# Performance work log

Hardware: AMD Instinct MI355X
Metric: run time of the kernel (lower is better)

## Reference

```python
import jax, jax.numpy as jnp
import numpy as np

B, H_HIST, S_DIM, HID, G, K, A = 1024, 16384, 32, 64, 10, 4, 8


def setup_inputs() -> dict:
    key = jax.random.key(0)
    ks = jax.random.split(key, 12)
    inp = {
        'state_batch': jax.random.normal(ks[0], (B, S_DIM), jnp.float32),
        'state_history_batch': jax.random.normal(ks[1], (H_HIST, S_DIM), jnp.float32),
        'joint_action_history_batch': jax.random.normal(ks[2], (H_HIST, G, A), jnp.float32),
        # per-abstract-agent encoder MLP: Linear(S->H) + ReLU, Linear(H->H) + ReLU, Linear(H->H) + ReLU
        'W0': jax.random.normal(ks[3], (K, S_DIM, HID), jnp.float32) / np.sqrt(S_DIM),
        'b0': jax.random.normal(ks[4], (K, HID), jnp.float32) * 0.01,
        'W1': jax.random.normal(ks[5], (K, HID, HID), jnp.float32) / np.sqrt(HID),
        'b1': jax.random.normal(ks[6], (K, HID), jnp.float32) * 0.01,
        'W2': jax.random.normal(ks[7], (K, HID, HID), jnp.float32) / np.sqrt(HID),
        'b2': jax.random.normal(ks[8], (K, HID), jnp.float32) * 0.01,
        'assignment_matrix': jnp.ones((G, K), jnp.float32),
    }
    return inp


def _encode(x, W0, b0, W1, b1, W2, b2):
    # x: [N, S_DIM] shared across K encoders -> [K, N, HID]
    h = jax.nn.relu(jnp.einsum('ni,kio->kno', x, W0) + b0[:, None, :])
    h = jax.nn.relu(jnp.einsum('kni,kio->kno', h, W1) + b1[:, None, :])
    h = jax.nn.relu(jnp.einsum('kni,kio->kno', h, W2) + b2[:, None, :])
    return h


def reference(state_batch, state_history_batch, joint_action_history_batch,
              W0, b0, W1, b1, W2, b2, assignment_matrix):
    enc_s = _encode(state_batch, W0, b0, W1, b1, W2, b2)            # [K, B, HID]
    enc_h = _encode(state_history_batch, W0, b0, W1, b1, W2, b2)    # [K, H, HID]
    # per (abstract agent k, batch item b): softmax over history of <enc_h, enc_s>
    attn = jax.nn.softmax(jnp.einsum('khd,kbd->kbh', enc_h, enc_s), axis=-1)  # [K, B, H]
    # weighted action aggregation: [H,G,A] contracted over H
    abs_pred = jnp.einsum('kbh,hga->kbga', attn, joint_action_history_batch)  # [K, B, G, A]
    soft_assign = jax.nn.softmax(assignment_matrix, axis=-1)                  # [G, K]
    out = jnp.einsum('gk,kbga->bga', soft_assign, abs_pred)                   # [B, G, A]
    return out
```

## Files before the change

### kernel.cpp

```cpp
#include <hip/hip_runtime.h>
#include <stdint.h>

#define B_SZ 1024
#define H_SZ 16384
#define SD   32
#define HID  64
#define G_SZ 10
#define K_SZ 4
#define A_SZ 8
#define VA   80
#define NC   16
#define CH   (H_SZ/NC)

typedef float f32x4  __attribute__((ext_vector_type(4)));
typedef short bf16x8 __attribute__((ext_vector_type(8)));

__device__ inline short f2bf(float a) {
    unsigned u = __float_as_uint(a);
    return (short)((u + 0x7FFFu + ((u >> 16) & 1u)) >> 16);
}
__device__ inline float bf2f(short s) {
    return __uint_as_float(((unsigned)(unsigned short)s) << 16);
}
__device__ inline void split_bf(float v, short& hi, short& lo) {
    hi = f2bf(v);
    lo = f2bf(v - bf2f(hi));
}
__device__ inline int pk_bf16(float a, float b) {
    unsigned ua = __float_as_uint(a), ub = __float_as_uint(b);
    ua = (ua + 0x7FFFu + ((ua >> 16) & 1u)) >> 16;
    ub = (ub + 0x7FFFu + ((ub >> 16) & 1u)) >> 16;
    return (int)(ua | (ub << 16));
}

__global__ __launch_bounds__(256, 2) void k_encode(
    const float* __restrict__ state, const float* __restrict__ hist,
    const float* __restrict__ act,
    const float* __restrict__ W0, const float* __restrict__ b0,
    const float* __restrict__ W1, const float* __restrict__ b1,
    const float* __restrict__ W2, const float* __restrict__ b2,
    short* __restrict__ enc_s_h, short* __restrict__ enc_s_l,
    short* __restrict__ enc_h_h, short* __restrict__ enc_h_l,
    short* __restrict__ vt_h, short* __restrict__ vt_l)
{
    __shared__ __align__(16) short smem[28672];
    const int bid = blockIdx.x;
    const int t = threadIdx.x;

    if (bid >= 1088) {
        short* tile_h = smem;
        short* tile_l = smem + 10752;
        const int h0 = (bid - 1088) * 128;
        for (int i = 0; i < 40; ++i) {
            int idx = t + i * 256;
            float v = act[(size_t)h0 * VA + idx];
            int h = idx / VA, c = idx - h * VA;
            short hh, ll; split_bf(v, hh, ll);
            tile_h[h * 84 + c] = hh;
            tile_l[h * 84 + c] = ll;
        }
        __syncthreads();
        for (int i = 0; i < 5; ++i) {
            int j = t + i * 256;
            int va = j >> 4, hc = j & 15;
            union { short s[8]; uint4 v; } uh, ul;
            #pragma unroll
            for (int uu = 0; uu < 8; ++uu) {
                uh.s[uu] = tile_h[(hc * 8 + uu) * 84 + va];
                ul.s[uu] = tile_l[(hc * 8 + uu) * 84 + va];
            }
            *(uint4*)(vt_h + (size_t)va * H_SZ + h0 + hc * 8) = uh.v;
            *(uint4*)(vt_l + (size_t)va * H_SZ + h0 + hc * 8) = ul.v;
        }
        return;
    }

    const int k = bid / 272;
    const int tl = bid % 272;
    const float* X;
    short *dst_h, *dst_l;
    if (tl < 16) {
        X = state + (size_t)tl * 64 * SD;
        dst_h = enc_s_h + ((size_t)k * B_SZ + tl * 64) * HID;
        dst_l = enc_s_l + ((size_t)k * B_SZ + tl * 64) * HID;
    } else {
        X = hist + (size_t)(tl - 16) * 64 * SD;
        dst_h = enc_h_h + ((size_t)k * H_SZ + (tl - 16) * 64) * HID;
        dst_l = enc_h_l + ((size_t)k * H_SZ + (tl - 16) * 64) * HID;
    }

    short* xt_h  = smem;
    short* xt_l  = smem + 2560;
    short* wt0_h = smem + 5120;
    short* wt0_l = smem + 7680;
    short* hb2_h = smem;
    short* hb2_l = smem + 4608;
    short* wt1_h = smem + 10240;
    short* wt1_l = smem + 14848;
    short* hb1_h = smem + 19456;
    short* hb1_l = smem + 24064;
    short* wt2_h = smem + 19456;
    short* wt2_l = smem + 24064;

    const float* W0k = W0 + k * (SD * HID);
    const float* W1k = W1 + k * (HID * HID);
    const float* W2k = W2 + k * (HID * HID);

    {
        int r = t >> 2, c0 = (t & 3) * 8;
        const float* src = X + r * SD + c0;
        #pragma unroll
        for (int u = 0; u < 8; ++u) {
            short hh, ll; split_bf(src[u], hh, ll);
            xt_h[r * 40 + c0 + u] = hh;
            xt_l[r * 40 + c0 + u] = ll;
        }
    }
    {
        int i = t >> 3, j0 = (t & 7) * 8;
        #pragma unroll
        for (int u = 0; u < 8; ++u) {
            short hh, ll; split_bf(W0k[i * HID + j0 + u], hh, ll);
            wt0_h[(j0 + u) * 40 + i] = hh;
            wt0_l[(j0 + u) * 40 + i] = ll;
        }
    }
    {
        int i = t >> 2, j0 = (t & 3) * 16;
        #pragma unroll
        for (int u = 0; u < 16; ++u) {
            short hh, ll; split_bf(W1k[i * HID + j0 + u], hh, ll);
            wt1_h[(j0 + u) * 72 + i] = hh;
            wt1_l[(j0 + u) * 72 + i] = ll;
        }
    }
    __syncthreads();

    const int w = t >> 6, l15 = t & 15, quad = (t >> 4) & 3;
    const f32x4 fz = {0.f, 0.f, 0.f, 0.f};

    {
        bf16x8 xa_h = *(const bf16x8*)(xt_h + (w * 16 + l15) * 40 + quad * 8);
        bf16x8 xa_l = *(const bf16x8*)(xt_l + (w * 16 + l15) * 40 + quad * 8);
        const float* b0k = b0 + k * HID;
        #pragma unroll
        for (int tt = 0; tt < 4; ++tt) {
            bf16x8 wf_h = *(const bf16x8*)(wt0_h + (l15 + 16 * tt) * 40 + quad * 8);
            bf16x8 wf_l = *(const bf16x8*)(wt0_l + (l15 + 16 * tt) * 40 + quad * 8);
            f32x4 c = __builtin_amdgcn_mfma_f32_16x16x32_bf16(xa_h, wf_h, fz, 0, 0, 0);
            c = __builtin_amdgcn_mfma_f32_16x16x32_bf16(xa_l, wf_h, c, 0, 0, 0);
            c = __builtin_amdgcn_mfma_f32_16x16x32_bf16(xa_h, wf_l, c, 0, 0, 0);
            float bias = b0k[l15 + 16 * tt];
            #pragma unroll
            for (int r = 0; r < 4; ++r) {
                float f = fmaxf(c[r] + bias, 0.f);
                short hh, ll; split_bf(f, hh, ll);
                hb1_h[(w * 16 + quad * 4 + r) * 72 + l15 + 16 * tt] = hh;
                hb1_l[(w * 16 + quad * 4 + r) * 72 + l15 + 16 * tt] = ll;
            }
        }
    }
    __syncthreads();
    {
        bf16x8 ha0_h = *(const bf16x8*)(hb1_h + (w * 16 + l15) * 72 + quad * 8);
        bf16x8 ha0_l = *(const bf16x8*)(hb1_l + (w * 16 + l15) * 72 + quad * 8);
        bf16x8 ha1_h = *(const bf16x8*)(hb1_h + (w * 16 + l15) * 72 + 32 + quad * 8);
        bf16x8 ha1_l = *(const bf16x8*)(hb1_l + (w * 16 + l15) * 72 + 32 + quad * 8);
        const float* b1k = b1 + k * HID;
        #pragma unroll
        for (int tt = 0; tt < 4; ++tt) {
            bf16x8 wfa_h = *(const bf16x8*)(wt1_h + (l15 + 16 * tt) * 72 + quad * 8);
            bf16x8 wfa_l = *(const bf16x8*)(wt1_l + (l15 + 16 * tt) * 72 + quad * 8);
            bf16x8 wfb_h = *(const bf16x8*)(wt1_h + (l15 + 16 * tt) * 72 + 32 + quad * 8);
            bf16x8 wfb_l = *(const bf16x8*)(wt1_l + (l15 + 16 * tt) * 72 + 32 + quad * 8);
            f32x4 c = __builtin_amdgcn_mfma_f32_16x16x32_bf16(ha0_h, wfa_h, fz, 0, 0, 0);
            c = __builtin_amdgcn_mfma_f32_16x16x32_bf16(ha1_h, wfb_h, c, 0, 0, 0);
            c = __builtin_amdgcn_mfma_f32_16x16x32_bf16(ha0_l, wfa_h, c, 0, 0, 0);
            c = __builtin_amdgcn_mfma_f32_16x16x32_bf16(ha1_l, wfb_h, c, 0, 0, 0);
            c = __builtin_amdgcn_mfma_f32_16x16x32_bf16(ha0_h, wfa_l, c, 0, 0, 0);
            c = __builtin_amdgcn_mfma_f32_16x16x32_bf16(ha1_h, wfb_l, c, 0, 0, 0);
            float bias = b1k[l15 + 16 * tt];
            #pragma unroll
            for (int r = 0; r < 4; ++r) {
                float f = fmaxf(c[r] + bias, 0.f);
                short hh, ll; split_bf(f, hh, ll);
                hb2_h[(w * 16 + quad * 4 + r) * 72 + l15 + 16 * tt] = hh;
                hb2_l[(w * 16 + quad * 4 + r) * 72 + l15 + 16 * tt] = ll;
            }
        }
    }
    __syncthreads();
    {
        int i = t >> 2, j0 = (t & 3) * 16;
        #pragma unroll
        for (int u = 0; u < 16; ++u) {
            short hh, ll; split_bf(W2k[i * HID + j0 + u], hh, ll);
            wt2_h[(j0 + u) * 72 + i] = hh;
            wt2_l[(j0 + u) * 72 + i] = ll;
        }
    }
    __syncthreads();
    {
        bf16x8 ha0_h = *(const bf16x8*)(hb2_h + (w * 16 + l15) * 72 + quad * 8);
        bf16x8 ha0_l = *(const bf16x8*)(hb2_l + (w * 16 + l15) * 72 + quad * 8);
        bf16x8 ha1_h = *(const bf16x8*)(hb2_h + (w * 16 + l15) * 72 + 32 + quad * 8);
        bf16x8 ha1_l = *(const bf16x8*)(hb2_l + (w * 16 + l15) * 72 + 32 + quad * 8);
        const float* b2k = b2 + k * HID;
        #pragma unroll
        for (int tt = 0; tt < 4; ++tt) {
            bf16x8 wfa_h = *(const bf16x8*)(wt2_h + (l15 + 16 * tt) * 72 + quad * 8);
            bf16x8 wfa_l = *(const bf16x8*)(wt2_l + (l15 + 16 * tt) * 72 + quad * 8);
            bf16x8 wfb_h = *(const bf16x8*)(wt2_h + (l15 + 16 * tt) * 72 + 32 + quad * 8);
            bf16x8 wfb_l = *(const bf16x8*)(wt2_l + (l15 + 16 * tt) * 72 + 32 + quad * 8);
            f32x4 c = __builtin_amdgcn_mfma_f32_16x16x32_bf16(ha0_h, wfa_h, fz, 0, 0, 0);
            c = __builtin_amdgcn_mfma_f32_16x16x32_bf16(ha1_h, wfb_h, c, 0, 0, 0);
            c = __builtin_amdgcn_mfma_f32_16x16x32_bf16(ha0_l, wfa_h, c, 0, 0, 0);
            c = __builtin_amdgcn_mfma_f32_16x16x32_bf16(ha1_l, wfb_h, c, 0, 0, 0);
            c = __builtin_amdgcn_mfma_f32_16x16x32_bf16(ha0_h, wfa_l, c, 0, 0, 0);
            c = __builtin_amdgcn_mfma_f32_16x16x32_bf16(ha1_h, wfb_l, c, 0, 0, 0);
            float bias = b2k[l15 + 16 * tt];
            #pragma unroll
            for (int r = 0; r < 4; ++r) {
                float f = fmaxf(c[r] + bias, 0.f);
                short hh, ll; split_bf(f, hh, ll);
                dst_h[(w * 16 + quad * 4 + r) * HID + l15 + 16 * tt] = hh;
                dst_l[(w * 16 + quad * 4 + r) * HID + l15 + 16 * tt] = ll;
            }
        }
    }
}

__global__ __launch_bounds__(256, 2) void k_flash(
    const short* __restrict__ enc_s_h, const short* __restrict__ enc_s_l,
    const short* __restrict__ enc_h_h, const short* __restrict__ enc_h_l,
    const short* __restrict__ vth, const short* __restrict__ vtl,
    float* __restrict__ Pm, float* __restrict__ Pl, float* __restrict__ Pacc)
{
    __shared__ __align__(16) short kh_h[32 * 72];
    __shared__ __align__(16) short kh_l[32 * 72];
    __shared__ __align__(16) short vts_h[80 * 40];
    __shared__ __align__(16) short vts_l[80 * 40];

    const int bid = blockIdx.x;
    const int mtile = bid & 7, chunk = (bid >> 3) & 15, k = bid >> 7;
    const int t = threadIdx.x, w = t >> 6, l15 = t & 15, quad = (t >> 4) & 3;
    const short* ehk_h = enc_h_h + (size_t)k * H_SZ * HID;
    const short* ehk_l = enc_h_l + (size_t)k * H_SZ * HID;
    const int h_base = chunk * CH;
    const int q0 = mtile * 128 + w * 32;
    const float L2E = 1.44269504f;
    const f32x4 fz = {0.f, 0.f, 0.f, 0.f};

    bf16x8 qh[2][2], ql[2][2];
    #pragma unroll
    for (int sub = 0; sub < 2; ++sub)
        #pragma unroll
        for (int kb = 0; kb < 2; ++kb) {
            size_t off = ((size_t)k * B_SZ + q0 + sub * 16 + l15) * HID + kb * 32 + quad * 8;
            qh[sub][kb] = *(const bf16x8*)(enc_s_h + off);
            ql[sub][kb] = *(const bf16x8*)(enc_s_l + off);
        }

    f32x4 acc[2][5];
    #pragma unroll
    for (int s = 0; s < 2; ++s)
        #pragma unroll
        for (int tt = 0; tt < 5; ++tt) acc[s][tt] = fz;
    float mrun[2] = {-__builtin_inff(), -__builtin_inff()};
    float lrun[2] = {0.f, 0.f};

    const int krr = t >> 3, kcc = (t & 7) * 8;
    const int vrw = t >> 2, vcl = (t & 3) * 8;
    const int vrw2 = 64 + (t >> 2);

    uint4 pkh, pkl, pvh, pvl, pv2h, pv2l;
    auto load_tile = [&](int h0) {
        pkh = *(const uint4*)(ehk_h + (size_t)(h0 + krr) * HID + kcc);
        pkl = *(const uint4*)(ehk_l + (size_t)(h0 + krr) * HID + kcc);
        pvh = *(const uint4*)(vth + (size_t)vrw * H_SZ + h0 + vcl);
        pvl = *(const uint4*)(vtl + (size_t)vrw * H_SZ + h0 + vcl);
        if (t < 64) {
            pv2h = *(const uint4*)(vth + (size_t)vrw2 * H_SZ + h0 + vcl);
            pv2l = *(const uint4*)(vtl + (size_t)vrw2 * H_SZ + h0 + vcl);
        }
    };
    auto store_tile = [&]() {
        *(uint4*)(kh_h + krr * 72 + kcc) = pkh;
        *(uint4*)(kh_l + krr * 72 + kcc) = pkl;
        *(uint4*)(vts_h + vrw * 40 + vcl) = pvh;
        *(uint4*)(vts_l + vrw * 40 + vcl) = pvl;
        if (t < 64) {
            *(uint4*)(vts_h + vrw2 * 40 + vcl) = pv2h;
            *(uint4*)(vts_l + vrw2 * 40 + vcl) = pv2l;
        }
    };

    load_tile(h_base);
    store_tile();

    for (int it = 0; it < CH / 32; ++it) {
        const int h0 = h_base + it * 32;
        __syncthreads();
        if (it + 1 < CH / 32) load_tile(h0 + 32);

        bf16x8 ka_h[2][2], ka_l[2][2];
        #pragma unroll
        for (int hs = 0; hs < 2; ++hs)
            #pragma unroll
            for (int kb = 0; kb < 2; ++kb) {
                ka_h[hs][kb] = *(const bf16x8*)(kh_h + (hs * 16 + l15) * 72 + kb * 32 + quad * 8);
                ka_l[hs][kb] = *(const bf16x8*)(kh_l + (hs * 16 + l15) * 72 + kb * 32 + quad * 8);
            }

        bf16x8 pfv[2];
        #pragma unroll
        for (int sub = 0; sub < 2; ++sub) {
            f32x4 slo = __builtin_amdgcn_mfma_f32_16x16x32_bf16(ka_h[0][0], qh[sub][0], fz, 0, 0, 0);
            slo = __builtin_amdgcn_mfma_f32_16x16x32_bf16(ka_h[0][1], qh[sub][1], slo, 0, 0, 0);
            slo = __builtin_amdgcn_mfma_f32_16x16x32_bf16(ka_l[0][0], qh[sub][0], slo, 0, 0, 0);
            slo = __builtin_amdgcn_mfma_f32_16x16x32_bf16(ka_l[0][1], qh[sub][1], slo, 0, 0, 0);
            slo = __builtin_amdgcn_mfma_f32_16x16x32_bf16(ka_h[0][0], ql[sub][0], slo, 0, 0, 0);
            slo = __builtin_amdgcn_mfma_f32_16x16x32_bf16(ka_h[0][1], ql[sub][1], slo, 0, 0, 0);
            f32x4 shi = __builtin_amdgcn_mfma_f32_16x16x32_bf16(ka_h[1][0], qh[sub][0], fz, 0, 0, 0);
            shi = __builtin_amdgcn_mfma_f32_16x16x32_bf16(ka_h[1][1], qh[sub][1], shi, 0, 0, 0);
            shi = __builtin_amdgcn_mfma_f32_16x16x32_bf16(ka_l[1][0], qh[sub][0], shi, 0, 0, 0);
            shi = __builtin_amdgcn_mfma_f32_16x16x32_bf16(ka_l[1][1], qh[sub][1], shi, 0, 0, 0);
            shi = __builtin_amdgcn_mfma_f32_16x16x32_bf16(ka_h[1][0], ql[sub][0], shi, 0, 0, 0);
            shi = __builtin_amdgcn_mfma_f32_16x16x32_bf16(ka_h[1][1], ql[sub][1], shi, 0, 0, 0);

            float tm = fmaxf(fmaxf(fmaxf(slo[0], slo[1]), fmaxf(slo[2], slo[3])),
                             fmaxf(fmaxf(shi[0], shi[1]), fmaxf(shi[2], shi[3])));
            tm = fmaxf(tm, __shfl_xor(tm, 16));
            tm = fmaxf(tm, __shfl_xor(tm, 32));
            float mnew = fmaxf(mrun[sub], tm);
            float alpha = exp2f((mrun[sub] - mnew) * L2E);
            float p0 = exp2f((slo[0] - mnew) * L2E), p1 = exp2f((slo[1] - mnew) * L2E);
            float p2 = exp2f((slo[2] - mnew) * L2E), p3 = exp2f((slo[3] - mnew) * L2E);
            float p4 = exp2f((shi[0] - mnew) * L2E), p5 = exp2f((shi[1] - mnew) * L2E);
            float p6 = exp2f((shi[2] - mnew) * L2E), p7 = exp2f((shi[3] - mnew) * L2E);
            float ps = (p0 + p1) + (p2 + p3) + (p4 + p5) + (p6 + p7);
            ps += __shfl_xor(ps, 16);
            ps += __shfl_xor(ps, 32);
            lrun[sub] = lrun[sub] * alpha + ps;
            mrun[sub] = mnew;
            #pragma unroll
            for (int tt = 0; tt < 5; ++tt) acc[sub][tt] = acc[sub][tt] * alpha;

            int plo01 = pk_bf16(p0, p1), plo23 = pk_bf16(p2, p3);
            int phi01 = pk_bf16(p4, p5), phi23 = pk_bf16(p6, p7);
            union { int i[4]; bf16x8 v; } pf;
            #pragma unroll
            for (int jj = 0; jj < 4; ++jj) {
                int src = (((2 * quad + (jj >> 1)) & 3) << 4) + l15;
                int glo = __shfl((jj & 1) ? plo23 : plo01, src);
                int ghi = __shfl((jj & 1) ? phi23 : phi01, src);
                pf.i[jj] = (quad >= 2) ? ghi : glo;
            }
            pfv[sub] = pf.v;
        }

        #pragma unroll
        for (int tt = 0; tt < 5; ++tt) {
            bf16x8 vh = *(const bf16x8*)(vts_h + (l15 + 16 * tt) * 40 + quad * 8);
            bf16x8 vl = *(const bf16x8*)(vts_l + (l15 + 16 * tt) * 40 + quad * 8);
            acc[0][tt] = __builtin_amdgcn_mfma_f32_16x16x32_bf16(vh, pfv[0], acc[0][tt], 0, 0, 0);
            acc[0][tt] = __builtin_amdgcn_mfma_f32_16x16x32_bf16(vl, pfv[0], acc[0][tt], 0, 0, 0);
            acc[1][tt] = __builtin_amdgcn_mfma_f32_16x16x32_bf16(vh, pfv[1], acc[1][tt], 0, 0, 0);
            acc[1][tt] = __builtin_amdgcn_mfma_f32_16x16x32_bf16(vl, pfv[1], acc[1][tt], 0, 0, 0);
        }

        __syncthreads();
        if (it + 1 < CH / 32) store_tile();
    }

    const int qg = k * B_SZ + q0;
    #pragma unroll
    for (int sub = 0; sub < 2; ++sub) {
        int q = qg + sub * 16 + l15;
        if (quad == 0) {
            Pm[chunk * 4096 + q] = mrun[sub];
            Pl[chunk * 4096 + q] = lrun[sub];
        }
        #pragma unroll
        for (int tt = 0; tt < 5; ++tt)
            #pragma unroll
            for (int r = 0; r < 4; ++r) {
                int va = tt * 16 + quad * 4 + r;
                Pacc[((size_t)chunk * VA + va) * 4096 + q] = acc[sub][tt][r];
            }
    }
}

__global__ __launch_bounds__(256) void k_reduce1(
    const float* __restrict__ Pm, const float* __restrict__ Pl,
    const float* __restrict__ Pacc, float* __restrict__ O)
{
    const int bid = blockIdx.x;
    const int qb = bid / 5, vc = bid - qb * 5;
    const int t = threadIdx.x;
    const int q = qb * 64 + (t & 63);
    const int va0 = vc * 16 + (t >> 6) * 4;
    const float L2E = 1.44269504f;

    float mc[NC];
    float M = -__builtin_inff();
    #pragma unroll
    for (int c = 0; c < NC; ++c) { mc[c] = Pm[c * 4096 + q]; M = fmaxf(M, mc[c]); }
    float wv[NC];
    float L = 0.f;
    #pragma unroll
    for (int c = 0; c < NC; ++c) {
        wv[c] = exp2f((mc[c] - M) * L2E);
        L += wv[c] * Pl[c * 4096 + q];
    }
    float inv = 1.f / L;
    float o[4] = {0.f, 0.f, 0.f, 0.f};
    #pragma unroll
    for (int c = 0; c < NC; ++c) {
        #pragma unroll
        for (int j = 0; j < 4; ++j)
            o[j] += wv[c] * Pacc[((size_t)c * VA + va0 + j) * 4096 + q];
    }
    #pragma unroll
    for (int j = 0; j < 4; ++j)
        O[(size_t)q * VA + va0 + j] = o[j] * inv;
}

__global__ __launch_bounds__(256) void k_reduce2(
    const float* __restrict__ O, const float* __restrict__ assign,
    float* __restrict__ out)
{
    const int idx = blockIdx.x * 256 + threadIdx.x;
    const int b = idx / VA, va = idx - b * VA, g = va >> 3;
    const float L2E = 1.44269504f;
    float a0 = assign[g * K_SZ + 0], a1 = assign[g * K_SZ + 1];
    float a2 = assign[g * K_SZ + 2], a3 = assign[g * K_SZ + 3];
    float mx = fmaxf(fmaxf(a0, a1), fmaxf(a2, a3));
    float e0 = exp2f((a0 - mx) * L2E), e1 = exp2f((a1 - mx) * L2E);
    float e2 = exp2f((a2 - mx) * L2E), e3 = exp2f((a3 - mx) * L2E);
    float inv = 1.f / (e0 + e1 + e2 + e3);
    float o = e0 * O[((size_t)(0 * B_SZ + b)) * VA + va]
            + e1 * O[((size_t)(1 * B_SZ + b)) * VA + va]
            + e2 * O[((size_t)(2 * B_SZ + b)) * VA + va]
            + e3 * O[((size_t)(3 * B_SZ + b)) * VA + va];
    out[idx] = o * inv;
}

extern "C" void kernel_launch(void* const* d_in, const int* in_sizes, int n_in,
                              void* d_out, int out_size, void* d_ws, size_t ws_size,
                              hipStream_t stream)
{
    const float* state  = (const float*)d_in[0];
    const float* hist   = (const float*)d_in[1];
    const float* act    = (const float*)d_in[2];
    const float* W0     = (const float*)d_in[3];
    const float* b0     = (const float*)d_in[4];
    const float* W1     = (const float*)d_in[5];
    const float* b1     = (const float*)d_in[6];
    const float* W2     = (const float*)d_in[7];
    const float* b2     = (const float*)d_in[8];
    const float* assign = (const float*)d_in[9];
    float* out = (float*)d_out;

    char* ws = (char*)d_ws;
    short* enc_s_h = (short*)(ws);
    short* enc_s_l = (short*)(ws + 524288);
    short* enc_h_h = (short*)(ws + 1048576);
    short* enc_h_l = (short*)(ws + 9437184);
    short* vt_h    = (short*)(ws + 17825792);
    short* vt_l    = (short*)(ws + 20447232);
    float* Pm      = (float*)(ws + 23068672);
    float* Pl      = (float*)(ws + 23330816);
    float* Pacc    = (float*)(ws + 23592960);
    float* O       = (float*)(ws + 44564480);

    k_encode<<<1216, 256, 0, stream>>>(state, hist, act, W0, b0, W1, b1, W2, b2,
                                       enc_s_h, enc_s_l, enc_h_h, enc_h_l, vt_h, vt_l);
    k_flash<<<512, 256, 0, stream>>>(enc_s_h, enc_s_l, enc_h_h, enc_h_l, vt_h, vt_l,
                                     Pm, Pl, Pacc);
    k_reduce1<<<320, 256, 0, stream>>>(Pm, Pl, Pacc, O);
    k_reduce2<<<320, 256, 0, stream>>>(O, assign, out);
}
```

Baseline: 176.6 us.

## Precompute split bf16 weight blob and widen flash blocks to 512 threads

A new small kernel converts and transposes the encoder weights into a packed hi/lo bf16 blob once. k_encode then copies that blob into shared memory with vector loads instead of having each of its 1216 blocks redo the conversion. The flash kernel moves from 256 to 512 threads per block, with each wave owning 16 queries instead of 32. This halves per-wave registers and accumulators and spreads the tile loads across twice as many threads. The costs are one extra kernel launch, less reuse of each K/V tile per wave, and a changed launch-bounds occupancy target.

```diff
diff --git a/kernel.cpp b/kernel.cpp
--- a/kernel.cpp
+++ b/kernel.cpp
@@ -11,6 +11,7 @@
 #define VA   80
 #define NC   16
 #define CH   (H_SZ/NC)
+#define WBLOB_K 23552
 
 typedef float f32x4  __attribute__((ext_vector_type(4)));
 typedef short bf16x8 __attribute__((ext_vector_type(8)));
@@ -33,12 +34,37 @@
     return (int)(ua | (ub << 16));
 }
 
+__global__ __launch_bounds__(256) void k_prep(
+    const float* __restrict__ W0, const float* __restrict__ W1,
+    const float* __restrict__ W2, short* __restrict__ wblob)
+{
+    const int k = blockIdx.x, t = threadIdx.x;
+    const float* W0k = W0 + k * (SD * HID);
+    const float* W1k = W1 + k * (HID * HID);
+    const float* W2k = W2 + k * (HID * HID);
+    short* blob = wblob + (size_t)k * WBLOB_K;
+    for (int e = t; e < SD * HID; e += 256) {
+        int i = e >> 6, j = e & 63;
+        short hh, ll; split_bf(W0k[e], hh, ll);
+        blob[j * 40 + i] = hh;
+        blob[2560 + j * 40 + i] = ll;
+    }
+    for (int e = t; e < HID * HID; e += 256) {
+        int i = e >> 6, j = e & 63;
+        short hh, ll; split_bf(W1k[e], hh, ll);
+        blob[5120 + j * 72 + i] = hh;
+        blob[9728 + j * 72 + i] = ll;
+        short h2, l2; split_bf(W2k[e], h2, l2);
+        blob[14336 + j * 72 + i] = h2;
+        blob[18944 + j * 72 + i] = l2;
+    }
+}
+
 __global__ __launch_bounds__(256, 2) void k_encode(
     const float* __restrict__ state, const float* __restrict__ hist,
     const float* __restrict__ act,
-    const float* __restrict__ W0, const float* __restrict__ b0,
-    const float* __restrict__ W1, const float* __restrict__ b1,
-    const float* __restrict__ W2, const float* __restrict__ b2,
+    const float* __restrict__ b0, const float* __restrict__ b1,
+    const float* __restrict__ b2, const short* __restrict__ wblob,
     short* __restrict__ enc_s_h, short* __restrict__ enc_s_l,
     short* __restrict__ enc_h_h, short* __restrict__ enc_h_l,
     short* __restrict__ vt_h, short* __restrict__ vt_l)
@@ -91,10 +117,10 @@
 
     short* xt_h  = smem;
     short* xt_l  = smem + 2560;
+    short* hb2_h = smem;
+    short* hb2_l = smem + 4608;
     short* wt0_h = smem + 5120;
     short* wt0_l = smem + 7680;
-    short* hb2_h = smem;
-    short* hb2_l = smem + 4608;
     short* wt1_h = smem + 10240;
     short* wt1_l = smem + 14848;
     short* hb1_h = smem + 19456;
@@ -102,9 +128,7 @@
     short* wt2_h = smem + 19456;
     short* wt2_l = smem + 24064;
 
-    const float* W0k = W0 + k * (SD * HID);
-    const float* W1k = W1 + k * (HID * HID);
-    const float* W2k = W2 + k * (HID * HID);
+    const short* blob = wblob + (size_t)k * WBLOB_K;
 
     {
         int r = t >> 2, c0 = (t & 3) * 8;
@@ -117,22 +141,10 @@
         }
     }
     {
-        int i = t >> 3, j0 = (t & 7) * 8;
-        #pragma unroll
-        for (int u = 0; u < 8; ++u) {
-            short hh, ll; split_bf(W0k[i * HID + j0 + u], hh, ll);
-            wt0_h[(j0 + u) * 40 + i] = hh;
-            wt0_l[(j0 + u) * 40 + i] = ll;
-        }
-    }
-    {
-        int i = t >> 2, j0 = (t & 3) * 16;
-        #pragma unroll
-        for (int u = 0; u < 16; ++u) {
-            short hh, ll; split_bf(W1k[i * HID + j0 + u], hh, ll);
-            wt1_h[(j0 + u) * 72 + i] = hh;
-            wt1_l[(j0 + u) * 72 + i] = ll;
-        }
+        const uint4* src = (const uint4*)blob;
+        uint4* dst = (uint4*)(smem + 5120);
+        #pragma unroll
+        for (int j = t; j < 1792; j += 256) dst[j] = src[j];
     }
     __syncthreads();
 
@@ -191,13 +203,10 @@
     }
     __syncthreads();
     {
-        int i = t >> 2, j0 = (t & 3) * 16;
-        #pragma unroll
-        for (int u = 0; u < 16; ++u) {
-            short hh, ll; split_bf(W2k[i * HID + j0 + u], hh, ll);
-            wt2_h[(j0 + u) * 72 + i] = hh;
-            wt2_l[(j0 + u) * 72 + i] = ll;
-        }
+        const uint4* src = (const uint4*)(blob + 14336);
+        uint4* dst = (uint4*)(smem + 19456);
+        #pragma unroll
+        for (int j = t; j < 1152; j += 256) dst[j] = src[j];
     }
     __syncthreads();
     {
@@ -230,7 +239,7 @@
     }
 }
 
-__global__ __launch_bounds__(256, 2) void k_flash(
+__global__ __launch_bounds__(512, 4) void k_flash(
     const short* __restrict__ enc_s_h, const short* __restrict__ enc_s_l,
     const short* __restrict__ enc_h_h, const short* __restrict__ enc_h_l,
     const short* __restrict__ vth, const short* __restrict__ vtl,
@@ -247,52 +256,51 @@
     const short* ehk_h = enc_h_h + (size_t)k * H_SZ * HID;
     const short* ehk_l = enc_h_l + (size_t)k * H_SZ * HID;
     const int h_base = chunk * CH;
-    const int q0 = mtile * 128 + w * 32;
+    const int q0 = mtile * 128 + w * 16;
     const float L2E = 1.44269504f;
     const f32x4 fz = {0.f, 0.f, 0.f, 0.f};
 
-    bf16x8 qh[2][2], ql[2][2];
-    #pragma unroll
-    for (int sub = 0; sub < 2; ++sub)
-        #pragma unroll
-        for (int kb = 0; kb < 2; ++kb) {
-            size_t off = ((size_t)k * B_SZ + q0 + sub * 16 + l15) * HID + kb * 32 + quad * 8;
-            qh[sub][kb] = *(const bf16x8*)(enc_s_h + off);
-            ql[sub][kb] = *(const bf16x8*)(enc_s_l + off);
-        }
-
-    f32x4 acc[2][5];
-    #pragma unroll
-    for (int s = 0; s < 2; ++s)
-        #pragma unroll
-        for (int tt = 0; tt < 5; ++tt) acc[s][tt] = fz;
-    float mrun[2] = {-__builtin_inff(), -__builtin_inff()};
-    float lrun[2] = {0.f, 0.f};
-
-    const int krr = t >> 3, kcc = (t & 7) * 8;
-    const int vrw = t >> 2, vcl = (t & 3) * 8;
-    const int vrw2 = 64 + (t >> 2);
-
-    uint4 pkh, pkl, pvh, pvl, pv2h, pv2l;
+    bf16x8 qh[2], ql[2];
+    #pragma unroll
+    for (int kb = 0; kb < 2; ++kb) {
+        size_t off = ((size_t)k * B_SZ + q0 + l15) * HID + kb * 32 + quad * 8;
+        qh[kb] = *(const bf16x8*)(enc_s_h + off);
+        ql[kb] = *(const bf16x8*)(enc_s_l + off);
+    }
+
+    f32x4 acc[5];
+    #pragma unroll
+    for (int tt = 0; tt < 5; ++tt) acc[tt] = fz;
+    float mrun = -__builtin_inff();
+    float lrun = 0.f;
+
+    const int jk = t & 255, kbuf = t >> 8;
+    const int krr = jk >> 3, kcc = (jk & 7) * 8;
+    const short* ksrc = kbuf ? ehk_l : ehk_h;
+    short* kdst = kbuf ? kh_l : kh_h;
+    uint4 pk, pv1, pv2;
+
+    auto vload = [&](int j, uint4& d, int h0) {
+        int bl = j >= 320; int r = j - (bl ? 320 : 0);
+        int va = r >> 2, c = (r & 3) * 8;
+        const short* s = bl ? vtl : vth;
+        d = *(const uint4*)(s + (size_t)va * H_SZ + h0 + c);
+    };
+    auto vstore = [&](int j, const uint4& v) {
+        int bl = j >= 320; int r = j - (bl ? 320 : 0);
+        int va = r >> 2, c = (r & 3) * 8;
+        short* d = bl ? vts_l : vts_h;
+        *(uint4*)(d + va * 40 + c) = v;
+    };
     auto load_tile = [&](int h0) {
-        pkh = *(const uint4*)(ehk_h + (size_t)(h0 + krr) * HID + kcc);
-        pkl = *(const uint4*)(ehk_l + (size_t)(h0 + krr) * HID + kcc);
-        pvh = *(const uint4*)(vth + (size_t)vrw * H_SZ + h0 + vcl);
-        pvl = *(const uint4*)(vtl + (size_t)vrw * H_SZ + h0 + vcl);
-        if (t < 64) {
-            pv2h = *(const uint4*)(vth + (size_t)vrw2 * H_SZ + h0 + vcl);
-            pv2l = *(const uint4*)(vtl + (size_t)vrw2 * H_SZ + h0 + vcl);
-        }
+        pk = *(const uint4*)(ksrc + (size_t)(h0 + krr) * HID + kcc);
+        vload(t, pv1, h0);
+        if (t < 128) vload(512 + t, pv2, h0);
     };
     auto store_tile = [&]() {
-        *(uint4*)(kh_h + krr * 72 + kcc) = pkh;
-        *(uint4*)(kh_l + krr * 72 + kcc) = pkl;
-        *(uint4*)(vts_h + vrw * 40 + vcl) = pvh;
-        *(uint4*)(vts_l + vrw * 40 + vcl) = pvl;
-        if (t < 64) {
-            *(uint4*)(vts_h + vrw2 * 40 + vcl) = pv2h;
-            *(uint4*)(vts_l + vrw2 * 40 + vcl) = pv2l;
-        }
+        *(uint4*)(kdst + krr * 72 + kcc) = pk;
+        vstore(t, pv1);
+        if (t < 128) vstore(512 + t, pv2);
     };
 
     load_tile(h_base);
@@ -312,83 +320,72 @@
                 ka_l[hs][kb] = *(const bf16x8*)(kh_l + (hs * 16 + l15) * 72 + kb * 32 + quad * 8);
             }
 
-        bf16x8 pfv[2];
-        #pragma unroll
-        for (int sub = 0; sub < 2; ++sub) {
-            f32x4 slo = __builtin_amdgcn_mfma_f32_16x16x32_bf16(ka_h[0][0], qh[sub][0], fz, 0, 0, 0);
-            slo = __builtin_amdgcn_mfma_f32_16x16x32_bf16(ka_h[0][1], qh[sub][1], slo, 0, 0, 0);
-            slo = __builtin_amdgcn_mfma_f32_16x16x32_bf16(ka_l[0][0], qh[sub][0], slo, 0, 0, 0);
-            slo = __builtin_amdgcn_mfma_f32_16x16x32_bf16(ka_l[0][1], qh[sub][1], slo, 0, 0, 0);
-            slo = __builtin_amdgcn_mfma_f32_16x16x32_bf16(ka_h[0][0], ql[sub][0], slo, 0, 0, 0);
-            slo = __builtin_amdgcn_mfma_f32_16x16x32_bf16(ka_h[0][1], ql[sub][1], slo, 0, 0, 0);
-            f32x4 shi = __builtin_amdgcn_mfma_f32_16x16x32_bf16(ka_h[1][0], qh[sub][0], fz, 0, 0, 0);
-            shi = __builtin_amdgcn_mfma_f32_16x16x32_bf16(ka_h[1][1], qh[sub][1], shi, 0, 0, 0);
-            shi = __builtin_amdgcn_mfma_f32_16x16x32_bf16(ka_l[1][0], qh[sub][0], shi, 0, 0, 0);
-            shi = __builtin_amdgcn_mfma_f32_16x16x32_bf16(ka_l[1][1], qh[sub][1], shi, 0, 0, 0);
-            shi = __builtin_amdgcn_mfma_f32_16x16x32_bf16(ka_h[1][0], ql[sub][0], shi, 0, 0, 0);
-            shi = __builtin_amdgcn_mfma_f32_16x16x32_bf16(ka_h[1][1], ql[sub][1], shi, 0, 0, 0);
-
-            float tm = fmaxf(fmaxf(fmaxf(slo[0], slo[1]), fmaxf(slo[2], slo[3])),
-                             fmaxf(fmaxf(shi[0], shi[1]), fmaxf(shi[2], shi[3])));
-            tm = fmaxf(tm, __shfl_xor(tm, 16));
-            tm = fmaxf(tm, __shfl_xor(tm, 32));
-            float mnew = fmaxf(mrun[sub], tm);
-            float alpha = exp2f((mrun[sub] - mnew) * L2E);
-            float p0 = exp2f((slo[0] - mnew) * L2E), p1 = exp2f((slo[1] - mnew) * L2E);
-            float p2 = exp2f((slo[2] - mnew) * L2E), p3 = exp2f((slo[3] - mnew) * L2E);
-            float p4 = exp2f((shi[0] - mnew) * L2E), p5 = exp2f((shi[1] - mnew) * L2E);
-            float p6 = exp2f((shi[2] - mnew) * L2E), p7 = exp2f((shi[3] - mnew) * L2E);
-            float ps = (p0 + p1) + (p2 + p3) + (p4 + p5) + (p6 + p7);
-            ps += __shfl_xor(ps, 16);
-            ps += __shfl_xor(ps, 32);
-            lrun[sub] = lrun[sub] * alpha + ps;
-            mrun[sub] = mnew;
-            #pragma unroll
-            for (int tt = 0; tt < 5; ++tt) acc[sub][tt] = acc[sub][tt] * alpha;
-
-            int plo01 = pk_bf16(p0, p1), plo23 = pk_bf16(p2, p3);
-            int phi01 = pk_bf16(p4, p5), phi23 = pk_bf16(p6, p7);
-            union { int i[4]; bf16x8 v; } pf;
-            #pragma unroll
-            for (int jj = 0; jj < 4; ++jj) {
-                int src = (((2 * quad + (jj >> 1)) & 3) << 4) + l15;
-                int glo = __shfl((jj & 1) ? plo23 : plo01, src);
-                int ghi = __shfl((jj & 1) ? phi23 : phi01, src);
-                pf.i[jj] = (quad >= 2) ? ghi : glo;
-            }
-            pfv[sub] = pf.v;
+        f32x4 slo = __builtin_amdgcn_mfma_f32_16x16x32_bf16(ka_h[0][0], qh[0], fz, 0, 0, 0);
+        slo = __builtin_amdgcn_mfma_f32_16x16x32_bf16(ka_h[0][1], qh[1], slo, 0, 0, 0);
+        slo = __builtin_amdgcn_mfma_f32_16x16x32_bf16(ka_l[0][0], qh[0], slo, 0, 0, 0);
+        slo = __builtin_amdgcn_mfma_f32_16x16x32_bf16(ka_l[0][1], qh[1], slo, 0, 0, 0);
+        slo = __builtin_amdgcn_mfma_f32_16x16x32_bf16(ka_h[0][0], ql[0], slo, 0, 0, 0);
+        slo = __builtin_amdgcn_mfma_f32_16x16x32_bf16(ka_h[0][1], ql[1], slo, 0, 0, 0);
+        f32x4 shi = __builtin_amdgcn_mfma_f32_16x16x32_bf16(ka_h[1][0], qh[0], fz, 0, 0, 0);
+        shi = __builtin_amdgcn_mfma_f32_16x16x32_bf16(ka_h[1][1], qh[1], shi, 0, 0, 0);
+        shi = __builtin_amdgcn_mfma_f32_16x16x32_bf16(ka_l[1][0], qh[0], shi, 0, 0, 0);
+        shi = __builtin_amdgcn_mfma_f32_16x16x32_bf16(ka_l[1][1], qh[1], shi, 0, 0, 0);
+        shi = __builtin_amdgcn_mfma_f32_16x16x32_bf16(ka_h[1][0], ql[0], shi, 0, 0, 0);
+        shi = __builtin_amdgcn_mfma_f32_16x16x32_bf16(ka_h[1][1], ql[1], shi, 0, 0, 0);
+
+        float tm = fmaxf(fmaxf(fmaxf(slo[0], slo[1]), fmaxf(slo[2], slo[3])),
+                         fmaxf(fmaxf(shi[0], shi[1]), fmaxf(shi[2], shi[3])));
+        tm = fmaxf(tm, __shfl_xor(tm, 16));
+        tm = fmaxf(tm, __shfl_xor(tm, 32));
+        float mnew = fmaxf(mrun, tm);
+        float alpha = exp2f((mrun - mnew) * L2E);
+        float p0 = exp2f((slo[0] - mnew) * L2E), p1 = exp2f((slo[1] - mnew) * L2E);
+        float p2 = exp2f((slo[2] - mnew) * L2E), p3 = exp2f((slo[3] - mnew) * L2E);
+        float p4 = exp2f((shi[0] - mnew) * L2E), p5 = exp2f((shi[1] - mnew) * L2E);
+        float p6 = exp2f((shi[2] - mnew) * L2E), p7 = exp2f((shi[3] - mnew) * L2E);
+        float ps = (p0 + p1) + (p2 + p3) + (p4 + p5) + (p6 + p7);
+        ps += __shfl_xor(ps, 16);
+        ps += __shfl_xor(ps, 32);
+        lrun = lrun * alpha + ps;
+        mrun = mnew;
+        #pragma unroll
+        for (int tt = 0; tt < 5; ++tt) acc[tt] = acc[tt] * alpha;
+
+        int plo01 = pk_bf16(p0, p1), plo23 = pk_bf16(p2, p3);
+        int phi01 = pk_bf16(p4, p5), phi23 = pk_bf16(p6, p7);
+        union { int i[4]; bf16x8 v; } pf;
+        #pragma unroll
+        for (int jj = 0; jj < 4; ++jj) {
+            int src = (((2 * quad + (jj >> 1)) & 3) << 4) + l15;
+            int glo = __shfl((jj & 1) ? plo23 : plo01, src);
+            int ghi = __shfl((jj & 1) ? phi23 : phi01, src);
+            pf.i[jj] = (quad >= 2) ? ghi : glo;
         }
 
         #pragma unroll
         for (int tt = 0; tt < 5; ++tt) {
             bf16x8 vh = *(const bf16x8*)(vts_h + (l15 + 16 * tt) * 40 + quad * 8);
             bf16x8 vl = *(const bf16x8*)(vts_l + (l15 + 16 * tt) * 40 + quad * 8);
-            acc[0][tt] = __builtin_amdgcn_mfma_f32_16x16x32_bf16(vh, pfv[0], acc[0][tt], 0, 0, 0);
-            acc[0][tt] = __builtin_amdgcn_mfma_f32_16x16x32_bf16(vl, pfv[0], acc[0][tt], 0, 0, 0);
-            acc[1][tt] = __builtin_amdgcn_mfma_f32_16x16x32_bf16(vh, pfv[1], acc[1][tt], 0, 0, 0);
-            acc[1][tt] = __builtin_amdgcn_mfma_f32_16x16x32_bf16(vl, pfv[1], acc[1][tt], 0, 0, 0);
+            acc[tt] = __builtin_amdgcn_mfma_f32_16x16x32_bf16(vh, pf.v, acc[tt], 0, 0, 0);
+            acc[tt] = __builtin_amdgcn_mfma_f32_16x16x32_bf16(vl, pf.v, acc[tt], 0, 0, 0);
         }
 
         __syncthreads();
         if (it + 1 < CH / 32) store_tile();
     }
 
-    const int qg = k * B_SZ + q0;
-    #pragma unroll
-    for (int sub = 0; sub < 2; ++sub) {
-        int q = qg + sub * 16 + l15;
-        if (quad == 0) {
-            Pm[chunk * 4096 + q] = mrun[sub];
-            Pl[chunk * 4096 + q] = lrun[sub];
-        }
-        #pragma unroll
-        for (int tt = 0; tt < 5; ++tt)
-            #pragma unroll
-            for (int r = 0; r < 4; ++r) {
-                int va = tt * 16 + quad * 4 + r;
-                Pacc[((size_t)chunk * VA + va) * 4096 + q] = acc[sub][tt][r];
-            }
-    }
+    const int q = k * B_SZ + q0 + l15;
+    if (quad == 0) {
+        Pm[chunk * 4096 + q] = mrun;
+        Pl[chunk * 4096 + q] = lrun;
+    }
+    #pragma unroll
+    for (int tt = 0; tt < 5; ++tt)
+        #pragma unroll
+        for (int r = 0; r < 4; ++r) {
+            int va = tt * 16 + quad * 4 + r;
+            Pacc[((size_t)chunk * VA + va) * 4096 + q] = acc[tt][r];
+        }
 }
 
 __global__ __launch_bounds__(256) void k_reduce1(
@@ -469,14 +466,16 @@
     short* enc_h_l = (short*)(ws + 9437184);
     short* vt_h    = (short*)(ws + 17825792);
     short* vt_l    = (short*)(ws + 20447232);
-    float* Pm      = (float*)(ws + 23068672);
-    float* Pl      = (float*)(ws + 23330816);
-    float* Pacc    = (float*)(ws + 23592960);
-    float* O       = (float*)(ws + 44564480);
-
-    k_encode<<<1216, 256, 0, stream>>>(state, hist, act, W0, b0, W1, b1, W2, b2,
+    short* wblob   = (short*)(ws + 23068672);
+    float* Pm      = (float*)(ws + 23257088);
+    float* Pl      = (float*)(ws + 23519232);
+    float* Pacc    = (float*)(ws + 23781376);
+    float* O       = (float*)(ws + 44752896);
+
+    k_prep<<<4, 256, 0, stream>>>(W0, W1, W2, wblob);
+    k_encode<<<1216, 256, 0, stream>>>(state, hist, act, b0, b1, b2, wblob,
                                        enc_s_h, enc_s_l, enc_h_h, enc_h_l, vt_h, vt_l);
-    k_flash<<<512, 256, 0, stream>>>(enc_s_h, enc_s_l, enc_h_h, enc_h_l, vt_h, vt_l,
+    k_flash<<<512, 512, 0, stream>>>(enc_s_h, enc_s_l, enc_h_h, enc_h_l, vt_h, vt_l,
                                      Pm, Pl, Pacc);
     k_reduce1<<<320, 256, 0, stream>>>(Pm, Pl, Pacc, O);
     k_reduce2<<<320, 256, 0, stream>>>(O, assign, out);
```

New measurement: 192.3 us. 8.9% more time.

## Fuse reduce kernels, swap MFMA operands for packed stores, remap flash grid

Applied to the files above, without the earlier changes.

Merges the two reduction kernels into one that combines the flash partials per k and applies the assignment softmax directly, removing the intermediate O buffer and one launch. In the encoder, MFMA operands are swapped so each lane holds four consecutive output columns, which allows vectorized bias loads and packed 64-bit LDS/global stores instead of scalar short stores. The flash kernel block index mapping is changed so consecutive blocks cover different k/chunk pairs of the same mtile, which may change L2 locality. The fused reduce recomputes the Pm/Pl merge once per va, adding redundant exp work.

```diff
diff --git a/kernel.cpp b/kernel.cpp
--- a/kernel.cpp
+++ b/kernel.cpp
@@ -31,6 +31,9 @@
     ua = (ua + 0x7FFFu + ((ua >> 16) & 1u)) >> 16;
     ub = (ub + 0x7FFFu + ((ub >> 16) & 1u)) >> 16;
     return (int)(ua | (ub << 16));
+}
+__device__ inline unsigned pks(short a, short b) {
+    return (unsigned)(unsigned short)a | ((unsigned)(unsigned short)b << 16);
 }
 
 __global__ __launch_bounds__(256, 2) void k_encode(
@@ -91,10 +94,10 @@
 
     short* xt_h  = smem;
     short* xt_l  = smem + 2560;
+    short* hb2_h = smem;
+    short* hb2_l = smem + 4608;
     short* wt0_h = smem + 5120;
     short* wt0_l = smem + 7680;
-    short* hb2_h = smem;
-    short* hb2_l = smem + 4608;
     short* wt1_h = smem + 10240;
     short* wt1_l = smem + 14848;
     short* hb1_h = smem + 19456;
@@ -110,10 +113,12 @@
         int r = t >> 2, c0 = (t & 3) * 8;
         const float* src = X + r * SD + c0;
         #pragma unroll
-        for (int u = 0; u < 8; ++u) {
-            short hh, ll; split_bf(src[u], hh, ll);
-            xt_h[r * 40 + c0 + u] = hh;
-            xt_l[r * 40 + c0 + u] = ll;
+        for (int u = 0; u < 4; ++u) {
+            short h0s, l0s, h1s, l1s;
+            split_bf(src[2 * u], h0s, l0s);
+            split_bf(src[2 * u + 1], h1s, l1s);
+            *(unsigned*)(xt_h + r * 40 + c0 + 2 * u) = pks(h0s, h1s);
+            *(unsigned*)(xt_l + r * 40 + c0 + 2 * u) = pks(l0s, l1s);
         }
     }
     {
@@ -147,17 +152,19 @@
         for (int tt = 0; tt < 4; ++tt) {
             bf16x8 wf_h = *(const bf16x8*)(wt0_h + (l15 + 16 * tt) * 40 + quad * 8);
             bf16x8 wf_l = *(const bf16x8*)(wt0_l + (l15 + 16 * tt) * 40 + quad * 8);
-            f32x4 c = __builtin_amdgcn_mfma_f32_16x16x32_bf16(xa_h, wf_h, fz, 0, 0, 0);
-            c = __builtin_amdgcn_mfma_f32_16x16x32_bf16(xa_l, wf_h, c, 0, 0, 0);
-            c = __builtin_amdgcn_mfma_f32_16x16x32_bf16(xa_h, wf_l, c, 0, 0, 0);
-            float bias = b0k[l15 + 16 * tt];
-            #pragma unroll
-            for (int r = 0; r < 4; ++r) {
-                float f = fmaxf(c[r] + bias, 0.f);
-                short hh, ll; split_bf(f, hh, ll);
-                hb1_h[(w * 16 + quad * 4 + r) * 72 + l15 + 16 * tt] = hh;
-                hb1_l[(w * 16 + quad * 4 + r) * 72 + l15 + 16 * tt] = ll;
-            }
+            f32x4 c = __builtin_amdgcn_mfma_f32_16x16x32_bf16(wf_h, xa_h, fz, 0, 0, 0);
+            c = __builtin_amdgcn_mfma_f32_16x16x32_bf16(wf_h, xa_l, c, 0, 0, 0);
+            c = __builtin_amdgcn_mfma_f32_16x16x32_bf16(wf_l, xa_h, c, 0, 0, 0);
+            const float4 bb = *(const float4*)(b0k + 16 * tt + quad * 4);
+            float f0 = fmaxf(c[0] + bb.x, 0.f), f1 = fmaxf(c[1] + bb.y, 0.f);
+            float f2 = fmaxf(c[2] + bb.z, 0.f), f3 = fmaxf(c[3] + bb.w, 0.f);
+            short h0s,l0s,h1s,l1s,h2s,l2s,h3s,l3s;
+            split_bf(f0,h0s,l0s); split_bf(f1,h1s,l1s);
+            split_bf(f2,h2s,l2s); split_bf(f3,h3s,l3s);
+            uint2 uh = { pks(h0s,h1s), pks(h2s,h3s) };
+            uint2 ul = { pks(l0s,l1s), pks(l2s,l3s) };
+            *(uint2*)(hb1_h + (w * 16 + l15) * 72 + 16 * tt + quad * 4) = uh;
+            *(uint2*)(hb1_l + (w * 16 + l15) * 72 + 16 * tt + quad * 4) = ul;
         }
     }
     __syncthreads();
@@ -173,20 +180,22 @@
             bf16x8 wfa_l = *(const bf16x8*)(wt1_l + (l15 + 16 * tt) * 72 + quad * 8);
             bf16x8 wfb_h = *(const bf16x8*)(wt1_h + (l15 + 16 * tt) * 72 + 32 + quad * 8);
             bf16x8 wfb_l = *(const bf16x8*)(wt1_l + (l15 + 16 * tt) * 72 + 32 + quad * 8);
-            f32x4 c = __builtin_amdgcn_mfma_f32_16x16x32_bf16(ha0_h, wfa_h, fz, 0, 0, 0);
-            c = __builtin_amdgcn_mfma_f32_16x16x32_bf16(ha1_h, wfb_h, c, 0, 0, 0);
-            c = __builtin_amdgcn_mfma_f32_16x16x32_bf16(ha0_l, wfa_h, c, 0, 0, 0);
-            c = __builtin_amdgcn_mfma_f32_16x16x32_bf16(ha1_l, wfb_h, c, 0, 0, 0);
-            c = __builtin_amdgcn_mfma_f32_16x16x32_bf16(ha0_h, wfa_l, c, 0, 0, 0);
-            c = __builtin_amdgcn_mfma_f32_16x16x32_bf16(ha1_h, wfb_l, c, 0, 0, 0);
-            float bias = b1k[l15 + 16 * tt];
-            #pragma unroll
-            for (int r = 0; r < 4; ++r) {
-                float f = fmaxf(c[r] + bias, 0.f);
-                short hh, ll; split_bf(f, hh, ll);
-                hb2_h[(w * 16 + quad * 4 + r) * 72 + l15 + 16 * tt] = hh;
-                hb2_l[(w * 16 + quad * 4 + r) * 72 + l15 + 16 * tt] = ll;
-            }
+            f32x4 c = __builtin_amdgcn_mfma_f32_16x16x32_bf16(wfa_h, ha0_h, fz, 0, 0, 0);
+            c = __builtin_amdgcn_mfma_f32_16x16x32_bf16(wfb_h, ha1_h, c, 0, 0, 0);
+            c = __builtin_amdgcn_mfma_f32_16x16x32_bf16(wfa_h, ha0_l, c, 0, 0, 0);
+            c = __builtin_amdgcn_mfma_f32_16x16x32_bf16(wfb_h, ha1_l, c, 0, 0, 0);
+            c = __builtin_amdgcn_mfma_f32_16x16x32_bf16(wfa_l, ha0_h, c, 0, 0, 0);
+            c = __builtin_amdgcn_mfma_f32_16x16x32_bf16(wfb_l, ha1_h, c, 0, 0, 0);
+            const float4 bb = *(const float4*)(b1k + 16 * tt + quad * 4);
+            float f0 = fmaxf(c[0] + bb.x, 0.f), f1 = fmaxf(c[1] + bb.y, 0.f);
+            float f2 = fmaxf(c[2] + bb.z, 0.f), f3 = fmaxf(c[3] + bb.w, 0.f);
+            short h0s,l0s,h1s,l1s,h2s,l2s,h3s,l3s;
+            split_bf(f0,h0s,l0s); split_bf(f1,h1s,l1s);
+            split_bf(f2,h2s,l2s); split_bf(f3,h3s,l3s);
+            uint2 uh = { pks(h0s,h1s), pks(h2s,h3s) };
+            uint2 ul = { pks(l0s,l1s), pks(l2s,l3s) };
+            *(uint2*)(hb2_h + (w * 16 + l15) * 72 + 16 * tt + quad * 4) = uh;
+            *(uint2*)(hb2_l + (w * 16 + l15) * 72 + 16 * tt + quad * 4) = ul;
         }
     }
     __syncthreads();
@@ -212,20 +221,22 @@
             bf16x8 wfa_l = *(const bf16x8*)(wt2_l + (l15 + 16 * tt) * 72 + quad * 8);
             bf16x8 wfb_h = *(const bf16x8*)(wt2_h + (l15 + 16 * tt) * 72 + 32 + quad * 8);
             bf16x8 wfb_l = *(const bf16x8*)(wt2_l + (l15 + 16 * tt) * 72 + 32 + quad * 8);
-            f32x4 c = __builtin_amdgcn_mfma_f32_16x16x32_bf16(ha0_h, wfa_h, fz, 0, 0, 0);
-            c = __builtin_amdgcn_mfma_f32_16x16x32_bf16(ha1_h, wfb_h, c, 0, 0, 0);
-            c = __builtin_amdgcn_mfma_f32_16x16x32_bf16(ha0_l, wfa_h, c, 0, 0, 0);
-            c = __builtin_amdgcn_mfma_f32_16x16x32_bf16(ha1_l, wfb_h, c, 0, 0, 0);
-            c = __builtin_amdgcn_mfma_f32_16x16x32_bf16(ha0_h, wfa_l, c, 0, 0, 0);
-            c = __builtin_amdgcn_mfma_f32_16x16x32_bf16(ha1_h, wfb_l, c, 0, 0, 0);
-            float bias = b2k[l15 + 16 * tt];
-            #pragma unroll
-            for (int r = 0; r < 4; ++r) {
-                float f = fmaxf(c[r] + bias, 0.f);
-                short hh, ll; split_bf(f, hh, ll);
-                dst_h[(w * 16 + quad * 4 + r) * HID + l15 + 16 * tt] = hh;
-                dst_l[(w * 16 + quad * 4 + r) * HID + l15 + 16 * tt] = ll;
-            }
+            f32x4 c = __builtin_amdgcn_mfma_f32_16x16x32_bf16(wfa_h, ha0_h, fz, 0, 0, 0);
+            c = __builtin_amdgcn_mfma_f32_16x16x32_bf16(wfb_h, ha1_h, c, 0, 0, 0);
+            c = __builtin_amdgcn_mfma_f32_16x16x32_bf16(wfa_h, ha0_l, c, 0, 0, 0);
+            c = __builtin_amdgcn_mfma_f32_16x16x32_bf16(wfb_h, ha1_l, c, 0, 0, 0);
+            c = __builtin_amdgcn_mfma_f32_16x16x32_bf16(wfa_l, ha0_h, c, 0, 0, 0);
+            c = __builtin_amdgcn_mfma_f32_16x16x32_bf16(wfb_l, ha1_h, c, 0, 0, 0);
+            const float4 bb = *(const float4*)(b2k + 16 * tt + quad * 4);
+            float f0 = fmaxf(c[0] + bb.x, 0.f), f1 = fmaxf(c[1] + bb.y, 0.f);
+            float f2 = fmaxf(c[2] + bb.z, 0.f), f3 = fmaxf(c[3] + bb.w, 0.f);
+            short h0s,l0s,h1s,l1s,h2s,l2s,h3s,l3s;
+            split_bf(f0,h0s,l0s); split_bf(f1,h1s,l1s);
+            split_bf(f2,h2s,l2s); split_bf(f3,h3s,l3s);
+            uint2 uh = { pks(h0s,h1s), pks(h2s,h3s) };
+            uint2 ul = { pks(l0s,l1s), pks(l2s,l3s) };
+            *(uint2*)(dst_h + (w * 16 + l15) * HID + 16 * tt + quad * 4) = uh;
+            *(uint2*)(dst_l + (w * 16 + l15) * HID + 16 * tt + quad * 4) = ul;
         }
     }
 }
@@ -242,7 +253,9 @@
     __shared__ __align__(16) short vts_l[80 * 40];
 
     const int bid = blockIdx.x;
-    const int mtile = bid & 7, chunk = (bid >> 3) & 15, k = bid >> 7;
+    const int group = bid & 63;
+    const int mtile = bid >> 6;
+    const int chunk = group >> 2, k = group & 3;
     const int t = threadIdx.x, w = t >> 6, l15 = t & 15, quad = (t >> 4) & 3;
     const short* ehk_h = enc_h_h + (size_t)k * H_SZ * HID;
     const short* ehk_l = enc_h_l + (size_t)k * H_SZ * HID;
@@ -391,59 +404,45 @@
     }
 }
 
-__global__ __launch_bounds__(256) void k_reduce1(
+__global__ __launch_bounds__(256) void k_reduce(
     const float* __restrict__ Pm, const float* __restrict__ Pl,
-    const float* __restrict__ Pacc, float* __restrict__ O)
+    const float* __restrict__ Pacc, const float* __restrict__ assign,
+    float* __restrict__ out)
 {
     const int bid = blockIdx.x;
-    const int qb = bid / 5, vc = bid - qb * 5;
+    const int qb = bid / 20, vc = bid - qb * 20;
     const int t = threadIdx.x;
-    const int q = qb * 64 + (t & 63);
-    const int va0 = vc * 16 + (t >> 6) * 4;
+    const int b = qb * 64 + (t & 63);
+    const int va = vc * 4 + (t >> 6);
+    const int g = va >> 3;
     const float L2E = 1.44269504f;
 
-    float mc[NC];
-    float M = -__builtin_inff();
-    #pragma unroll
-    for (int c = 0; c < NC; ++c) { mc[c] = Pm[c * 4096 + q]; M = fmaxf(M, mc[c]); }
-    float wv[NC];
-    float L = 0.f;
-    #pragma unroll
-    for (int c = 0; c < NC; ++c) {
-        wv[c] = exp2f((mc[c] - M) * L2E);
-        L += wv[c] * Pl[c * 4096 + q];
-    }
-    float inv = 1.f / L;
-    float o[4] = {0.f, 0.f, 0.f, 0.f};
-    #pragma unroll
-    for (int c = 0; c < NC; ++c) {
-        #pragma unroll
-        for (int j = 0; j < 4; ++j)
-            o[j] += wv[c] * Pacc[((size_t)c * VA + va0 + j) * 4096 + q];
-    }
-    #pragma unroll
-    for (int j = 0; j < 4; ++j)
-        O[(size_t)q * VA + va0 + j] = o[j] * inv;
-}
-
-__global__ __launch_bounds__(256) void k_reduce2(
-    const float* __restrict__ O, const float* __restrict__ assign,
-    float* __restrict__ out)
-{
-    const int idx = blockIdx.x * 256 + threadIdx.x;
-    const int b = idx / VA, va = idx - b * VA, g = va >> 3;
-    const float L2E = 1.44269504f;
     float a0 = assign[g * K_SZ + 0], a1 = assign[g * K_SZ + 1];
     float a2 = assign[g * K_SZ + 2], a3 = assign[g * K_SZ + 3];
     float mx = fmaxf(fmaxf(a0, a1), fmaxf(a2, a3));
-    float e0 = exp2f((a0 - mx) * L2E), e1 = exp2f((a1 - mx) * L2E);
-    float e2 = exp2f((a2 - mx) * L2E), e3 = exp2f((a3 - mx) * L2E);
-    float inv = 1.f / (e0 + e1 + e2 + e3);
-    float o = e0 * O[((size_t)(0 * B_SZ + b)) * VA + va]
-            + e1 * O[((size_t)(1 * B_SZ + b)) * VA + va]
-            + e2 * O[((size_t)(2 * B_SZ + b)) * VA + va]
-            + e3 * O[((size_t)(3 * B_SZ + b)) * VA + va];
-    out[idx] = o * inv;
+    float ek[4];
+    ek[0] = exp2f((a0 - mx) * L2E); ek[1] = exp2f((a1 - mx) * L2E);
+    ek[2] = exp2f((a2 - mx) * L2E); ek[3] = exp2f((a3 - mx) * L2E);
+    float inv_se = 1.f / (ek[0] + ek[1] + ek[2] + ek[3]);
+
+    float res = 0.f;
+    #pragma unroll
+    for (int k = 0; k < 4; ++k) {
+        const int q = k * B_SZ + b;
+        float mc[NC];
+        float M = -__builtin_inff();
+        #pragma unroll
+        for (int c = 0; c < NC; ++c) { mc[c] = Pm[c * 4096 + q]; M = fmaxf(M, mc[c]); }
+        float L = 0.f, o = 0.f;
+        #pragma unroll
+        for (int c = 0; c < NC; ++c) {
+            float wv = exp2f((mc[c] - M) * L2E);
+            L += wv * Pl[c * 4096 + q];
+            o += wv * Pacc[((size_t)c * VA + va) * 4096 + q];
+        }
+        res += ek[k] * o / L;
+    }
+    out[(size_t)b * VA + va] = res * inv_se;
 }
 
 extern "C" void kernel_launch(void* const* d_in, const int* in_sizes, int n_in,
@@ -472,12 +471,10 @@
     float* Pm      = (float*)(ws + 23068672);
     float* Pl      = (float*)(ws + 23330816);
     float* Pacc    = (float*)(ws + 23592960);
-    float* O       = (float*)(ws + 44564480);
 
     k_encode<<<1216, 256, 0, stream>>>(state, hist, act, W0, b0, W1, b1, W2, b2,
                                        enc_s_h, enc_s_l, enc_h_h, enc_h_l, vt_h, vt_l);
     k_flash<<<512, 256, 0, stream>>>(enc_s_h, enc_s_l, enc_h_h, enc_h_l, vt_h, vt_l,
                                      Pm, Pl, Pacc);
-    k_reduce1<<<320, 256, 0, stream>>>(Pm, Pl, Pacc, O);
-    k_reduce2<<<320, 256, 0, stream>>>(O, assign, out);
-}
+    k_reduce<<<320, 256, 0, stream>>>(Pm, Pl, Pacc, assign, out);
+}
```

Measured after the change: 178.5 us. About the same (+1.1%).
